# Kernel optimization log

Measured on AMD Instinct MI355X. Metric: run time of the kernel, lower is better.

## Reference

```python
import jax, jax.numpy as jnp
import numpy as np

LOWER = 300  # hidden size of the critic MLP


def setup_inputs() -> dict:
    key = jax.random.key(0)
    ks = jax.random.split(key, 6)
    N, XD, YD = 1024, 768, 768
    x = jax.random.normal(ks[0], (N, XD), dtype=jnp.float32)
    y = jax.random.normal(ks[1], (N, YD), dtype=jnp.float32)
    # Linear(x_dim+y_dim -> LOWER), Linear(LOWER -> 1); Kaiming-uniform-ish init
    b1_lim = 1.0 / np.sqrt(XD + YD)
    b2_lim = 1.0 / np.sqrt(LOWER)
    W1 = jax.random.uniform(ks[2], (XD + YD, LOWER), jnp.float32, -b1_lim, b1_lim)
    b1 = jax.random.uniform(ks[3], (LOWER,), jnp.float32, -b1_lim, b1_lim)
    W2 = jax.random.uniform(ks[4], (LOWER, 1), jnp.float32, -b2_lim, b2_lim)
    b2 = jax.random.uniform(ks[5], (1,), jnp.float32, -b2_lim, b2_lim)
    return {"x_samples": x, "y_samples": y, "W1": W1, "b1": b1, "W2": W2, "b2": b2}


def reference(x_samples, y_samples, W1, b1, W2, b2):
    N = y_samples.shape[0]
    xd = x_samples.shape[-1]
    # Decompose first Linear: cat([x, y]) @ W1 == x @ W1[:xd] + y @ W1[xd:]
    Wx, Wy = W1[:xd], W1[xd:]
    hx = x_samples @ Wx          # [N, LOWER]
    hy = y_samples @ Wy          # [N, LOWER]
    w2 = W2[:, 0]                # [LOWER]

    def critic(h):
        # relu -> Linear(LOWER->1) -> softplus
        return jax.nn.softplus(jax.nn.relu(h) @ w2 + b2[0])

    # T0[i] = F(x[i], y[i])
    T0 = critic(hx + hy + b1)                       # [N]
    # T1[i, j] = F(x[j], y[i])  (x tiled over dim 0, y over dim 1)
    h_pair = hy[:, None, :] + hx[None, :, :] + b1   # [N, N, LOWER]
    T1 = critic(h_pair)                             # [N, N]
    lower_bound = (T0.mean()
                   - jax.nn.logsumexp(T1, axis=1).mean()
                   - jnp.log(jnp.float32(N)))
    return lower_bound
```

## Files before the change

### kernel.cpp

```cpp
#include <hip/hip_runtime.h>
#include <math.h>

#define N_S 1024
#define XD  768
#define LOW 300
#define KP  320
#define KP2 160

typedef _Float16 h2  __attribute__((ext_vector_type(2)));
typedef __fp16   g2  __attribute__((ext_vector_type(2)));
typedef _Float16 v8h __attribute__((ext_vector_type(8)));
typedef float    f4  __attribute__((ext_vector_type(4)));

union U32H2 { unsigned int u; h2 h; };
__device__ inline h2 u2h(unsigned int v){ U32H2 t; t.u = v; return t.h; }
__device__ inline unsigned int pk(float a, float b){
    g2 t = __builtin_amdgcn_cvt_pkrtz(a, b);
    return __builtin_bit_cast(unsigned int, t);
}
union U4V8 { uint4 u; v8h v; };

#define STR 34

__global__ __launch_bounds__(512)
void gemm_h(const float* __restrict__ x, const float* __restrict__ y,
            const float* __restrict__ W1, const float* __restrict__ b1g,
            _Float16* __restrict__ hx_h, _Float16* __restrict__ hy_h)
{
    const int which = blockIdx.z;
    const float* A = which ? y : x;
    const float* W = W1 + (size_t)which * XD * LOW;
    _Float16* out = which ? hy_h : hx_h;

    const int n0 = blockIdx.x * 64;
    const int r0 = blockIdx.y * 64;

    __shared__ unsigned int As[2][64][STR];
    __shared__ unsigned int Bs[2][64][STR];

    const int tid = threadIdx.x;
    const int w = tid >> 6, l = tid & 63;
    const int wn = w >> 1, wm = w & 1;
    const int lr = l & 15, lg = l >> 4;

    const int arow = tid >> 3, aq = tid & 7;
    const int bn = tid & 63, bms = tid >> 6;
    const bool bin = (n0 + bn) < LOW;

    f4 acc[2] = {};

    float4 a0, a1; float bw[8];
    a0 = *(const float4*)&A[(size_t)(r0 + arow) * XD + aq * 8];
    a1 = *(const float4*)&A[(size_t)(r0 + arow) * XD + aq * 8 + 4];
    #pragma unroll
    for (int s = 0; s < 8; ++s)
        bw[s] = bin ? W[(size_t)(bms * 8 + s) * LOW + n0 + bn] : 0.f;

    const int NC = XD / 64;
    for (int c = 0; c < NC; ++c) {
        const int buf = c & 1;
        {
            uint4 pa = { pk(a0.x,a0.y), pk(a0.z,a0.w), pk(a1.x,a1.y), pk(a1.z,a1.w) };
            *(uint4*)&As[buf][arow][aq * 4] = pa;
            uint4 pb = { pk(bw[0],bw[1]), pk(bw[2],bw[3]), pk(bw[4],bw[5]), pk(bw[6],bw[7]) };
            *(uint4*)&Bs[buf][bn][bms * 4] = pb;
        }
        __syncthreads();
        if (c + 1 < NC) {
            const int kb = (c + 1) * 64;
            a0 = *(const float4*)&A[(size_t)(r0 + arow) * XD + kb + aq * 8];
            a1 = *(const float4*)&A[(size_t)(r0 + arow) * XD + kb + aq * 8 + 4];
            #pragma unroll
            for (int s = 0; s < 8; ++s)
                bw[s] = bin ? W[(size_t)(kb + bms * 8 + s) * LOW + n0 + bn] : 0.f;
        }
        #pragma unroll
        for (int ks = 0; ks < 2; ++ks) {
            const int ko = ks * 16 + lg * 4;
            U4V8 bf; bf.u = *(const uint4*)&Bs[buf][wn * 16 + lr][ko];
            #pragma unroll
            for (int mt = 0; mt < 2; ++mt) {
                U4V8 af; af.u = *(const uint4*)&As[buf][wm * 32 + mt * 16 + lr][ko];
                acc[mt] = __builtin_amdgcn_mfma_f32_16x16x32_f16(af.v, bf.v, acc[mt], 0, 0, 0);
            }
        }
    }

    const int col = n0 + wn * 16 + lr;
    const float b1v = (which && col < LOW) ? b1g[col] : 0.f;
    #pragma unroll
    for (int mt = 0; mt < 2; ++mt)
        #pragma unroll
        for (int r = 0; r < 4; ++r) {
            const int row = r0 + wm * 32 + mt * 16 + lg * 4 + r;
            out[(size_t)row * KP + col] = (_Float16)(acc[mt][r] + b1v);
        }
}

__global__ __launch_bounds__(256)
void pair_kernel(const unsigned int* __restrict__ hx_h, const unsigned int* __restrict__ hy_h,
                 const float* __restrict__ W2, const float* __restrict__ b2,
                 float* __restrict__ part, float* __restrict__ diag)
{
    const int j0 = blockIdx.x * 64;
    const int i0 = blockIdx.y * 32;
    const int jb = blockIdx.x;

    __shared__ unsigned int Hy[2][16][36];
    __shared__ unsigned int Hx[2][16][66];
    __shared__ unsigned int w2s[KP2];

    const int tid = threadIdx.x;
    const int tx = tid & 31;
    const int ty = tid >> 5;

    if (tid < KP2) {
        int k = tid * 2;
        float w0 = (k < LOW) ? W2[k] : 0.f;
        float w1 = (k + 1 < LOW) ? W2[k + 1] : 0.f;
        U32H2 p; p.h = h2{(_Float16)w0, (_Float16)w1};
        w2s[tid] = p.u;
    }

    const int yi = tid >> 3, yq = tid & 7;
    const int xj = tid >> 2, xq = tid & 3;

    uint2 ga  = *(const uint2*)&hy_h[(size_t)(i0 + yi) * KP2 + 2 * yq];
    uint2 gb0 = *(const uint2*)&hx_h[(size_t)(j0 + xj) * KP2 + 4 * xq];
    uint2 gb1 = *(const uint2*)&hx_h[(size_t)(j0 + xj) * KP2 + 4 * xq + 2];

    float acc[4][2] = {};
    const h2 hz = h2{(_Float16)0.f, (_Float16)0.f};

    const int NC = KP2 / 16;
    for (int c = 0; c < NC; ++c) {
        const int buf = c & 1;
        Hy[buf][2 * yq][yi]     = ga.x;
        Hy[buf][2 * yq + 1][yi] = ga.y;
        Hx[buf][4 * xq][xj]     = gb0.x;
        Hx[buf][4 * xq + 1][xj] = gb0.y;
        Hx[buf][4 * xq + 2][xj] = gb1.x;
        Hx[buf][4 * xq + 3][xj] = gb1.y;
        __syncthreads();
        if (c + 1 < NC) {
            const int kb = (c + 1) * 16;
            ga  = *(const uint2*)&hy_h[(size_t)(i0 + yi) * KP2 + kb + 2 * yq];
            gb0 = *(const uint2*)&hx_h[(size_t)(j0 + xj) * KP2 + kb + 4 * xq];
            gb1 = *(const uint2*)&hx_h[(size_t)(j0 + xj) * KP2 + kb + 4 * xq + 2];
        }
        #pragma unroll
        for (int kk = 0; kk < 16; ++kk) {
            const uint4 ya = *(const uint4*)&Hy[buf][kk][ty * 4];
            const uint2 xb = *(const uint2*)&Hx[buf][kk][tx * 2];
            const h2 w  = u2h(w2s[c * 16 + kk]);
            const h2 x0 = u2h(xb.x), x1 = u2h(xb.y);
            const unsigned int yar[4] = {ya.x, ya.y, ya.z, ya.w};
            #pragma unroll
            for (int r = 0; r < 4; ++r) {
                const h2 a = u2h(yar[r]);
                h2 z0 = __builtin_elementwise_max(a + x0, hz);
                h2 z1 = __builtin_elementwise_max(a + x1, hz);
                acc[r][0] = __builtin_amdgcn_fdot2(z0, w, acc[r][0], false);
                acc[r][1] = __builtin_amdgcn_fdot2(z1, w, acc[r][1], false);
            }
        }
    }

    const float b2v = b2[0];
    #pragma unroll
    for (int r = 0; r < 4; ++r) {
        const int row = i0 + ty * 4 + r;
        float s0 = acc[r][0] + b2v, s1 = acc[r][1] + b2v;
        float sp0 = fmaxf(s0, 0.f) + __logf(1.f + __expf(-fabsf(s0)));
        float sp1 = fmaxf(s1, 0.f) + __logf(1.f + __expf(-fabsf(s1)));
        const int c0 = j0 + tx * 2;
        if (c0 == row)     diag[row] = sp0;
        if (c0 + 1 == row) diag[row] = sp1;
        float es = __expf(sp0) + __expf(sp1);
        #pragma unroll
        for (int o = 1; o <= 16; o <<= 1) es += __shfl_xor(es, o, 64);
        if ((tid & 31) == 0) part[(size_t)row * 16 + jb] = es;
    }
}

__global__ __launch_bounds__(1024)
void lse_final(const float* __restrict__ part, const float* __restrict__ diag,
               float* __restrict__ out)
{
    const int i = threadIdx.x;
    const float4* p = (const float4*)(part + (size_t)i * 16);
    float s = 0.f;
    #pragma unroll
    for (int q = 0; q < 4; ++q) {
        float4 v = p[q];
        s += (v.x + v.y) + (v.z + v.w);
    }
    float c = diag[i] - __logf(s);

    #pragma unroll
    for (int o = 32; o > 0; o >>= 1) c += __shfl_xor(c, o, 64);
    __shared__ float ss[16];
    const int wid = i >> 6, lane = i & 63;
    if (lane == 0) ss[wid] = c;
    __syncthreads();
    if (i == 0) {
        float t = 0.f;
        #pragma unroll
        for (int q = 0; q < 16; ++q) t += ss[q];
        out[0] = t * (1.0f / N_S) - logf((float)N_S);
    }
}

extern "C" void kernel_launch(void* const* d_in, const int* in_sizes, int n_in,
                              void* d_out, int out_size, void* d_ws, size_t ws_size,
                              hipStream_t stream)
{
    const float* x  = (const float*)d_in[0];
    const float* y  = (const float*)d_in[1];
    const float* W1 = (const float*)d_in[2];
    const float* b1 = (const float*)d_in[3];
    const float* W2 = (const float*)d_in[4];
    const float* b2 = (const float*)d_in[5];
    float* out = (float*)d_out;

    unsigned int* hx_h = (unsigned int*)d_ws;
    unsigned int* hy_h = hx_h + (size_t)N_S * KP2;
    float* part = (float*)(hy_h + (size_t)N_S * KP2);
    float* diag = part + (size_t)N_S * 16;

    dim3 g1(5, 16, 2);
    gemm_h<<<g1, 512, 0, stream>>>(x, y, W1, b1,
                                   (_Float16*)hx_h, (_Float16*)hy_h);

    dim3 g2(16, 32);
    pair_kernel<<<g2, 256, 0, stream>>>(hx_h, hy_h, W2, b2, part, diag);

    lse_final<<<1, 1024, 0, stream>>>(part, diag, out);
}
```

Baseline: 41.85 us.

## Enlarge pair tile to 64x64 and fold softplus-exp identity into LSE

The pair kernel now computes a 64x64 output tile per block with a 4x4 register micro-tile per thread, staging hx/hy as uint2 pairs in shared memory and reading W2 directly from global into registers per chunk. It uses the identity exp(softplus(s)) = 1 + exp(s), so each element needs one exp instead of exp+log+exp, and the constant N is added back in the final reduction. Softplus is evaluated only on diagonal elements. This cuts transcendental work and raises arithmetic intensity per shared load. The cost is more register pressure from the larger tile, and fewer blocks in the grid.

```diff
diff --git a/kernel.cpp b/kernel.cpp
--- a/kernel.cpp
+++ b/kernel.cpp
@@ -97,71 +97,80 @@
         }
 }
 
+#define NCH 10
 __global__ __launch_bounds__(256)
 void pair_kernel(const unsigned int* __restrict__ hx_h, const unsigned int* __restrict__ hy_h,
                  const float* __restrict__ W2, const float* __restrict__ b2,
                  float* __restrict__ part, float* __restrict__ diag)
 {
-    const int j0 = blockIdx.x * 64;
-    const int i0 = blockIdx.y * 32;
-    const int jb = blockIdx.x;
-
-    __shared__ unsigned int Hy[2][16][36];
-    __shared__ unsigned int Hx[2][16][66];
-    __shared__ unsigned int w2s[KP2];
+    const int bx = blockIdx.x, by = blockIdx.y;
+    const int j0 = bx * 64, i0 = by * 64;
+
+    __shared__ uint2 Hy[2][8][68];
+    __shared__ uint2 Hx[2][8][68];
 
     const int tid = threadIdx.x;
-    const int tx = tid & 31;
-    const int ty = tid >> 5;
-
-    if (tid < KP2) {
-        int k = tid * 2;
-        float w0 = (k < LOW) ? W2[k] : 0.f;
-        float w1 = (k + 1 < LOW) ? W2[k + 1] : 0.f;
-        U32H2 p; p.h = h2{(_Float16)w0, (_Float16)w1};
-        w2s[tid] = p.u;
-    }
-
-    const int yi = tid >> 3, yq = tid & 7;
-    const int xj = tid >> 2, xq = tid & 3;
-
-    uint2 ga  = *(const uint2*)&hy_h[(size_t)(i0 + yi) * KP2 + 2 * yq];
-    uint2 gb0 = *(const uint2*)&hx_h[(size_t)(j0 + xj) * KP2 + 4 * xq];
-    uint2 gb1 = *(const uint2*)&hx_h[(size_t)(j0 + xj) * KP2 + 4 * xq + 2];
-
-    float acc[4][2] = {};
+    const int tx = tid & 15;
+    const int ty = tid >> 4;
+
+    const int srow = tid >> 2, skq = tid & 3;
+
+    const unsigned int* gy = &hy_h[(size_t)(i0 + srow) * KP2 + skq * 4];
+    const unsigned int* gx = &hx_h[(size_t)(j0 + srow) * KP2 + skq * 4];
+
+    uint4 ga = *(const uint4*)gy;
+    uint4 gb = *(const uint4*)gx;
+
+    float acc[4][4] = {};
     const h2 hz = h2{(_Float16)0.f, (_Float16)0.f};
 
-    const int NC = KP2 / 16;
-    for (int c = 0; c < NC; ++c) {
+    for (int c = 0; c < NCH; ++c) {
         const int buf = c & 1;
-        Hy[buf][2 * yq][yi]     = ga.x;
-        Hy[buf][2 * yq + 1][yi] = ga.y;
-        Hx[buf][4 * xq][xj]     = gb0.x;
-        Hx[buf][4 * xq + 1][xj] = gb0.y;
-        Hx[buf][4 * xq + 2][xj] = gb1.x;
-        Hx[buf][4 * xq + 3][xj] = gb1.y;
+        Hy[buf][skq*2  ][srow] = make_uint2(ga.x, ga.y);
+        Hy[buf][skq*2+1][srow] = make_uint2(ga.z, ga.w);
+        Hx[buf][skq*2  ][srow] = make_uint2(gb.x, gb.y);
+        Hx[buf][skq*2+1][srow] = make_uint2(gb.z, gb.w);
         __syncthreads();
-        if (c + 1 < NC) {
-            const int kb = (c + 1) * 16;
-            ga  = *(const uint2*)&hy_h[(size_t)(i0 + yi) * KP2 + kb + 2 * yq];
-            gb0 = *(const uint2*)&hx_h[(size_t)(j0 + xj) * KP2 + kb + 4 * xq];
-            gb1 = *(const uint2*)&hx_h[(size_t)(j0 + xj) * KP2 + kb + 4 * xq + 2];
-        }
-        #pragma unroll
-        for (int kk = 0; kk < 16; ++kk) {
-            const uint4 ya = *(const uint4*)&Hy[buf][kk][ty * 4];
-            const uint2 xb = *(const uint2*)&Hx[buf][kk][tx * 2];
-            const h2 w  = u2h(w2s[c * 16 + kk]);
-            const h2 x0 = u2h(xb.x), x1 = u2h(xb.y);
-            const unsigned int yar[4] = {ya.x, ya.y, ya.z, ya.w};
+        if (c + 1 < NCH) {
+            ga = *(const uint4*)(gy + (c + 1) * 16);
+            gb = *(const uint4*)(gx + (c + 1) * 16);
+        }
+
+        unsigned int wp[16];
+        {
+            const int kb = c * 32;
+            #pragma unroll
+            for (int t = 0; t < 8; ++t) {
+                float4 wv;
+                if (kb + t * 4 + 3 < LOW) wv = *(const float4*)&W2[kb + t * 4];
+                else wv = float4{0.f, 0.f, 0.f, 0.f};
+                wp[t * 2]     = pk(wv.x, wv.y);
+                wp[t * 2 + 1] = pk(wv.z, wv.w);
+            }
+        }
+
+        #pragma unroll
+        for (int kk2 = 0; kk2 < 8; ++kk2) {
+            uint2 ya[4], xb[4];
+            #pragma unroll
+            for (int r = 0; r < 4; ++r) ya[r] = Hy[buf][kk2][ty * 4 + r];
+            #pragma unroll
+            for (int q = 0; q < 4; ++q) xb[q] = Hx[buf][kk2][q * 16 + tx];
+            const h2 w0 = u2h(wp[kk2 * 2]);
+            const h2 w1 = u2h(wp[kk2 * 2 + 1]);
             #pragma unroll
             for (int r = 0; r < 4; ++r) {
-                const h2 a = u2h(yar[r]);
-                h2 z0 = __builtin_elementwise_max(a + x0, hz);
-                h2 z1 = __builtin_elementwise_max(a + x1, hz);
-                acc[r][0] = __builtin_amdgcn_fdot2(z0, w, acc[r][0], false);
-                acc[r][1] = __builtin_amdgcn_fdot2(z1, w, acc[r][1], false);
+                const h2 a0 = u2h(ya[r].x);
+                const h2 a1 = u2h(ya[r].y);
+                #pragma unroll
+                for (int q = 0; q < 4; ++q) {
+                    const h2 b0 = u2h(xb[q].x);
+                    const h2 b1 = u2h(xb[q].y);
+                    h2 z0 = __builtin_elementwise_max(a0 + b0, hz);
+                    h2 z1 = __builtin_elementwise_max(a1 + b1, hz);
+                    acc[r][q] = __builtin_amdgcn_fdot2(z0, w0, acc[r][q], false);
+                    acc[r][q] = __builtin_amdgcn_fdot2(z1, w1, acc[r][q], false);
+                }
             }
         }
     }
@@ -170,16 +179,18 @@
     #pragma unroll
     for (int r = 0; r < 4; ++r) {
         const int row = i0 + ty * 4 + r;
-        float s0 = acc[r][0] + b2v, s1 = acc[r][1] + b2v;
-        float sp0 = fmaxf(s0, 0.f) + __logf(1.f + __expf(-fabsf(s0)));
-        float sp1 = fmaxf(s1, 0.f) + __logf(1.f + __expf(-fabsf(s1)));
-        const int c0 = j0 + tx * 2;
-        if (c0 == row)     diag[row] = sp0;
-        if (c0 + 1 == row) diag[row] = sp1;
-        float es = __expf(sp0) + __expf(sp1);
-        #pragma unroll
-        for (int o = 1; o <= 16; o <<= 1) es += __shfl_xor(es, o, 64);
-        if ((tid & 31) == 0) part[(size_t)row * 16 + jb] = es;
+        float es = 0.f;
+        #pragma unroll
+        for (int q = 0; q < 4; ++q) {
+            const float s = acc[r][q] + b2v;
+            es += __expf(s);
+            const int col = j0 + q * 16 + tx;
+            if (col == row)
+                diag[row] = fmaxf(s, 0.f) + __logf(1.f + __expf(-fabsf(s)));
+        }
+        #pragma unroll
+        for (int o = 1; o <= 8; o <<= 1) es += __shfl_xor(es, o, 64);
+        if (tx == 0) part[(size_t)row * 16 + bx] = es;
     }
 }
 
@@ -195,7 +206,7 @@
         float4 v = p[q];
         s += (v.x + v.y) + (v.z + v.w);
     }
-    float c = diag[i] - __logf(s);
+    float c = diag[i] - __logf((float)N_S + s);
 
     #pragma unroll
     for (int o = 32; o > 0; o >>= 1) c += __shfl_xor(c, o, 64);
@@ -232,7 +243,7 @@
     gemm_h<<<g1, 512, 0, stream>>>(x, y, W1, b1,
                                    (_Float16*)hx_h, (_Float16*)hy_h);
 
-    dim3 g2(16, 32);
+    dim3 g2(16, 16);
     pair_kernel<<<g2, 256, 0, stream>>>(hx_h, hy_h, W2, b2, part, diag);
 
     lse_final<<<1, 1024, 0, stream>>>(part, diag, out);
```

New measurement: 44.31 us. 1.06x slower.

## Fuse GEMM, pair and LSE stages into one cooperative kernel

Applied to the files above, without the earlier changes.

Merges the three kernels into a single cooperative launch that separates the projection GEMM, pairwise critic and final reduction with grid-wide syncs, sharing LDS via a union. The GEMM is retiled to 32x64 blocks with 256 threads so all phases use the same block size. Softplus followed by exp is replaced algebraically by summing exp(s) and taking log(N + sum), removing transcendental work per pair. Risks include grid.sync overhead and, if the cooperative launch fails, a fallback three-kernel path.

```diff
diff --git a/kernel.cpp b/kernel.cpp
--- a/kernel.cpp
+++ b/kernel.cpp
@@ -1,11 +1,15 @@
 #include <hip/hip_runtime.h>
+#include <hip/hip_cooperative_groups.h>
 #include <math.h>
+
+namespace cg = cooperative_groups;
 
 #define N_S 1024
 #define XD  768
 #define LOW 300
 #define KP  320
 #define KP2 160
+#define GRID 512
 
 typedef _Float16 h2  __attribute__((ext_vector_type(2)));
 typedef __fp16   g2  __attribute__((ext_vector_type(2)));
@@ -20,27 +24,33 @@
 }
 union U4V8 { uint4 u; v8h v; };
 
-#define STR 34
-
-__global__ __launch_bounds__(512)
-void gemm_h(const float* __restrict__ x, const float* __restrict__ y,
-            const float* __restrict__ W1, const float* __restrict__ b1g,
-            _Float16* __restrict__ hx_h, _Float16* __restrict__ hy_h)
-{
-    const int which = blockIdx.z;
+struct SmemG {
+    unsigned int As[2][32][34];
+    unsigned int Bs[2][64][34];
+};
+struct SmemP {
+    unsigned int Hy[2][16][36];
+    unsigned int Hx[2][16][66];
+    unsigned int w2s[KP2];
+};
+union Smem { SmemG g; SmemP p; };
+
+__device__ void phase_gemm(Smem& sm, int job,
+    const float* __restrict__ x, const float* __restrict__ y,
+    const float* __restrict__ W1, const float* __restrict__ b1g,
+    unsigned int* __restrict__ hx_h, unsigned int* __restrict__ hy_h)
+{
+    const int tid = threadIdx.x;
+    const int which = job >= 160;
+    const int t = which ? job - 160 : job;
+    const int n0 = (t % 5) * 64;
+    const int r0 = (t / 5) * 32;
     const float* A = which ? y : x;
     const float* W = W1 + (size_t)which * XD * LOW;
-    _Float16* out = which ? hy_h : hx_h;
-
-    const int n0 = blockIdx.x * 64;
-    const int r0 = blockIdx.y * 64;
-
-    __shared__ unsigned int As[2][64][STR];
-    __shared__ unsigned int Bs[2][64][STR];
-
-    const int tid = threadIdx.x;
+    _Float16* outh = (_Float16*)(which ? hy_h : hx_h);
+
     const int w = tid >> 6, l = tid & 63;
-    const int wn = w >> 1, wm = w & 1;
+    const int wn = w & 1, wm = w >> 1;
     const int lr = l & 15, lg = l >> 4;
 
     const int arow = tid >> 3, aq = tid & 7;
@@ -48,111 +58,104 @@
     const bool bin = (n0 + bn) < LOW;
 
     f4 acc[2] = {};
-
-    float4 a0, a1; float bw[8];
+    float4 a0, a1; float bw[16];
     a0 = *(const float4*)&A[(size_t)(r0 + arow) * XD + aq * 8];
     a1 = *(const float4*)&A[(size_t)(r0 + arow) * XD + aq * 8 + 4];
     #pragma unroll
-    for (int s = 0; s < 8; ++s)
-        bw[s] = bin ? W[(size_t)(bms * 8 + s) * LOW + n0 + bn] : 0.f;
+    for (int s = 0; s < 16; ++s)
+        bw[s] = bin ? W[(size_t)(bms * 16 + s) * LOW + n0 + bn] : 0.f;
 
     const int NC = XD / 64;
     for (int c = 0; c < NC; ++c) {
         const int buf = c & 1;
-        {
-            uint4 pa = { pk(a0.x,a0.y), pk(a0.z,a0.w), pk(a1.x,a1.y), pk(a1.z,a1.w) };
-            *(uint4*)&As[buf][arow][aq * 4] = pa;
-            uint4 pb = { pk(bw[0],bw[1]), pk(bw[2],bw[3]), pk(bw[4],bw[5]), pk(bw[6],bw[7]) };
-            *(uint4*)&Bs[buf][bn][bms * 4] = pb;
-        }
+        *(uint4*)&sm.g.As[buf][arow][aq * 4] =
+            uint4{ pk(a0.x,a0.y), pk(a0.z,a0.w), pk(a1.x,a1.y), pk(a1.z,a1.w) };
+        *(uint4*)&sm.g.Bs[buf][bn][bms * 8] =
+            uint4{ pk(bw[0],bw[1]), pk(bw[2],bw[3]), pk(bw[4],bw[5]), pk(bw[6],bw[7]) };
+        *(uint4*)&sm.g.Bs[buf][bn][bms * 8 + 4] =
+            uint4{ pk(bw[8],bw[9]), pk(bw[10],bw[11]), pk(bw[12],bw[13]), pk(bw[14],bw[15]) };
         __syncthreads();
         if (c + 1 < NC) {
             const int kb = (c + 1) * 64;
             a0 = *(const float4*)&A[(size_t)(r0 + arow) * XD + kb + aq * 8];
             a1 = *(const float4*)&A[(size_t)(r0 + arow) * XD + kb + aq * 8 + 4];
             #pragma unroll
-            for (int s = 0; s < 8; ++s)
-                bw[s] = bin ? W[(size_t)(kb + bms * 8 + s) * LOW + n0 + bn] : 0.f;
+            for (int s = 0; s < 16; ++s)
+                bw[s] = bin ? W[(size_t)(kb + bms * 16 + s) * LOW + n0 + bn] : 0.f;
         }
         #pragma unroll
         for (int ks = 0; ks < 2; ++ks) {
             const int ko = ks * 16 + lg * 4;
-            U4V8 bf; bf.u = *(const uint4*)&Bs[buf][wn * 16 + lr][ko];
+            U4V8 af; af.u = *(const uint4*)&sm.g.As[buf][wm * 16 + lr][ko];
             #pragma unroll
-            for (int mt = 0; mt < 2; ++mt) {
-                U4V8 af; af.u = *(const uint4*)&As[buf][wm * 32 + mt * 16 + lr][ko];
-                acc[mt] = __builtin_amdgcn_mfma_f32_16x16x32_f16(af.v, bf.v, acc[mt], 0, 0, 0);
+            for (int nt = 0; nt < 2; ++nt) {
+                U4V8 bf; bf.u = *(const uint4*)&sm.g.Bs[buf][wn * 32 + nt * 16 + lr][ko];
+                acc[nt] = __builtin_amdgcn_mfma_f32_16x16x32_f16(af.v, bf.v, acc[nt], 0, 0, 0);
             }
         }
     }
 
-    const int col = n0 + wn * 16 + lr;
-    const float b1v = (which && col < LOW) ? b1g[col] : 0.f;
-    #pragma unroll
-    for (int mt = 0; mt < 2; ++mt)
+    #pragma unroll
+    for (int nt = 0; nt < 2; ++nt) {
+        const int col = n0 + wn * 32 + nt * 16 + lr;
+        const float b1v = (which && col < LOW) ? b1g[col] : 0.f;
         #pragma unroll
         for (int r = 0; r < 4; ++r) {
-            const int row = r0 + wm * 32 + mt * 16 + lg * 4 + r;
-            out[(size_t)row * KP + col] = (_Float16)(acc[mt][r] + b1v);
-        }
-}
-
-__global__ __launch_bounds__(256)
-void pair_kernel(const unsigned int* __restrict__ hx_h, const unsigned int* __restrict__ hy_h,
-                 const float* __restrict__ W2, const float* __restrict__ b2,
-                 float* __restrict__ part, float* __restrict__ diag)
-{
-    const int j0 = blockIdx.x * 64;
-    const int i0 = blockIdx.y * 32;
-    const int jb = blockIdx.x;
-
-    __shared__ unsigned int Hy[2][16][36];
-    __shared__ unsigned int Hx[2][16][66];
-    __shared__ unsigned int w2s[KP2];
-
+            const int row = r0 + wm * 16 + lg * 4 + r;
+            outh[(size_t)row * KP + col] = (_Float16)(acc[nt][r] + b1v);
+        }
+    }
+}
+
+__device__ void phase_pair(Smem& sm, int bid,
+    const unsigned int* __restrict__ hx_h, const unsigned int* __restrict__ hy_h,
+    const float* __restrict__ W2, const float* __restrict__ b2,
+    float* __restrict__ part, float* __restrict__ diag)
+{
     const int tid = threadIdx.x;
-    const int tx = tid & 31;
-    const int ty = tid >> 5;
+    const int jb = bid & 15, ib = bid >> 4;
+    const int j0 = jb * 64, i0 = ib * 32;
+    const int tx = tid & 31, ty = tid >> 5;
 
     if (tid < KP2) {
         int k = tid * 2;
         float w0 = (k < LOW) ? W2[k] : 0.f;
         float w1 = (k + 1 < LOW) ? W2[k + 1] : 0.f;
-        U32H2 p; p.h = h2{(_Float16)w0, (_Float16)w1};
-        w2s[tid] = p.u;
+        sm.p.w2s[tid] = pk(w0, w1);
     }
 
     const int yi = tid >> 3, yq = tid & 7;
     const int xj = tid >> 2, xq = tid & 3;
 
-    uint2 ga  = *(const uint2*)&hy_h[(size_t)(i0 + yi) * KP2 + 2 * yq];
-    uint2 gb0 = *(const uint2*)&hx_h[(size_t)(j0 + xj) * KP2 + 4 * xq];
-    uint2 gb1 = *(const uint2*)&hx_h[(size_t)(j0 + xj) * KP2 + 4 * xq + 2];
+    const unsigned int* gy = &hy_h[(size_t)(i0 + yi) * KP2 + 2 * yq];
+    const unsigned int* gx = &hx_h[(size_t)(j0 + xj) * KP2 + 4 * xq];
+    uint2 ga  = *(const uint2*)gy;
+    uint2 gb0 = *(const uint2*)gx;
+    uint2 gb1 = *(const uint2*)(gx + 2);
 
     float acc[4][2] = {};
     const h2 hz = h2{(_Float16)0.f, (_Float16)0.f};
 
-    const int NC = KP2 / 16;
-    for (int c = 0; c < NC; ++c) {
+    const int NCH = KP2 / 16;
+    for (int c = 0; c < NCH; ++c) {
         const int buf = c & 1;
-        Hy[buf][2 * yq][yi]     = ga.x;
-        Hy[buf][2 * yq + 1][yi] = ga.y;
-        Hx[buf][4 * xq][xj]     = gb0.x;
-        Hx[buf][4 * xq + 1][xj] = gb0.y;
-        Hx[buf][4 * xq + 2][xj] = gb1.x;
-        Hx[buf][4 * xq + 3][xj] = gb1.y;
+        sm.p.Hy[buf][2*yq  ][yi] = ga.x;
+        sm.p.Hy[buf][2*yq+1][yi] = ga.y;
+        sm.p.Hx[buf][4*xq  ][xj] = gb0.x;
+        sm.p.Hx[buf][4*xq+1][xj] = gb0.y;
+        sm.p.Hx[buf][4*xq+2][xj] = gb1.x;
+        sm.p.Hx[buf][4*xq+3][xj] = gb1.y;
         __syncthreads();
-        if (c + 1 < NC) {
-            const int kb = (c + 1) * 16;
-            ga  = *(const uint2*)&hy_h[(size_t)(i0 + yi) * KP2 + kb + 2 * yq];
-            gb0 = *(const uint2*)&hx_h[(size_t)(j0 + xj) * KP2 + kb + 4 * xq];
-            gb1 = *(const uint2*)&hx_h[(size_t)(j0 + xj) * KP2 + kb + 4 * xq + 2];
+        if (c + 1 < NCH) {
+            ga  = *(const uint2*)(gy + (c + 1) * 16);
+            gb0 = *(const uint2*)(gx + (c + 1) * 16);
+            gb1 = *(const uint2*)(gx + (c + 1) * 16 + 2);
         }
         #pragma unroll
         for (int kk = 0; kk < 16; ++kk) {
-            const uint4 ya = *(const uint4*)&Hy[buf][kk][ty * 4];
-            const uint2 xb = *(const uint2*)&Hx[buf][kk][tx * 2];
-            const h2 w  = u2h(w2s[c * 16 + kk]);
+            const uint4 ya = *(const uint4*)&sm.p.Hy[buf][kk][ty * 4];
+            const uint2 xb = *(const uint2*)&sm.p.Hx[buf][kk][tx * 2];
+            const h2 w  = u2h(sm.p.w2s[c * 16 + kk]);
             const h2 x0 = u2h(xb.x), x1 = u2h(xb.y);
             const unsigned int yar[4] = {ya.x, ya.y, ya.z, ya.w};
             #pragma unroll
@@ -171,44 +174,85 @@
     for (int r = 0; r < 4; ++r) {
         const int row = i0 + ty * 4 + r;
         float s0 = acc[r][0] + b2v, s1 = acc[r][1] + b2v;
-        float sp0 = fmaxf(s0, 0.f) + __logf(1.f + __expf(-fabsf(s0)));
-        float sp1 = fmaxf(s1, 0.f) + __logf(1.f + __expf(-fabsf(s1)));
         const int c0 = j0 + tx * 2;
-        if (c0 == row)     diag[row] = sp0;
-        if (c0 + 1 == row) diag[row] = sp1;
-        float es = __expf(sp0) + __expf(sp1);
+        if (c0 == row)     diag[row] = fmaxf(s0, 0.f) + __logf(1.f + __expf(-fabsf(s0)));
+        if (c0 + 1 == row) diag[row] = fmaxf(s1, 0.f) + __logf(1.f + __expf(-fabsf(s1)));
+        float es = __expf(s0) + __expf(s1);
         #pragma unroll
         for (int o = 1; o <= 16; o <<= 1) es += __shfl_xor(es, o, 64);
-        if ((tid & 31) == 0) part[(size_t)row * 16 + jb] = es;
-    }
-}
-
-__global__ __launch_bounds__(1024)
-void lse_final(const float* __restrict__ part, const float* __restrict__ diag,
-               float* __restrict__ out)
-{
-    const int i = threadIdx.x;
-    const float4* p = (const float4*)(part + (size_t)i * 16);
-    float s = 0.f;
-    #pragma unroll
-    for (int q = 0; q < 4; ++q) {
-        float4 v = p[q];
-        s += (v.x + v.y) + (v.z + v.w);
-    }
-    float c = diag[i] - __logf(s);
-
-    #pragma unroll
-    for (int o = 32; o > 0; o >>= 1) c += __shfl_xor(c, o, 64);
-    __shared__ float ss[16];
-    const int wid = i >> 6, lane = i & 63;
-    if (lane == 0) ss[wid] = c;
+        if (tx == 0) part[(size_t)row * 16 + jb] = es;
+    }
+}
+
+__device__ void phase_lse(const float* __restrict__ part,
+                          const float* __restrict__ diag, float* __restrict__ out)
+{
+    __shared__ float ssum[4];
+    const int tid = threadIdx.x;
+    float csum = 0.f;
+    #pragma unroll
+    for (int g = 0; g < 4; ++g) {
+        const int row = g * 256 + tid;
+        const float4* p = (const float4*)(part + (size_t)row * 16);
+        float s = 0.f;
+        #pragma unroll
+        for (int q = 0; q < 4; ++q) {
+            float4 v = p[q];
+            s += (v.x + v.y) + (v.z + v.w);
+        }
+        csum += diag[row] - __logf((float)N_S + s);
+    }
+    #pragma unroll
+    for (int o = 32; o > 0; o >>= 1) csum += __shfl_xor(csum, o, 64);
+    if ((tid & 63) == 0) ssum[tid >> 6] = csum;
     __syncthreads();
-    if (i == 0) {
-        float t = 0.f;
-        #pragma unroll
-        for (int q = 0; q < 16; ++q) t += ss[q];
-        out[0] = t * (1.0f / N_S) - logf((float)N_S);
-    }
+    if (tid == 0)
+        out[0] = (ssum[0] + ssum[1] + ssum[2] + ssum[3]) * (1.0f / N_S)
+               - logf((float)N_S);
+}
+
+__global__ __launch_bounds__(256)
+void fused(const float* __restrict__ x, const float* __restrict__ y,
+           const float* __restrict__ W1, const float* __restrict__ b1g,
+           const float* __restrict__ W2, const float* __restrict__ b2,
+           unsigned int* __restrict__ hx_h, unsigned int* __restrict__ hy_h,
+           float* __restrict__ part, float* __restrict__ diag,
+           float* __restrict__ out)
+{
+    __shared__ Smem sm;
+    cg::grid_group grid = cg::this_grid();
+    const int bid = blockIdx.x;
+
+    if (bid < 320)
+        phase_gemm(sm, bid, x, y, W1, b1g, hx_h, hy_h);
+    grid.sync();
+    phase_pair(sm, bid, hx_h, hy_h, W2, b2, part, diag);
+    grid.sync();
+    if (bid == 0)
+        phase_lse(part, diag, out);
+}
+
+__global__ __launch_bounds__(256)
+void gemm_k(const float* __restrict__ x, const float* __restrict__ y,
+            const float* __restrict__ W1, const float* __restrict__ b1g,
+            unsigned int* __restrict__ hx_h, unsigned int* __restrict__ hy_h)
+{
+    __shared__ Smem sm;
+    phase_gemm(sm, blockIdx.x, x, y, W1, b1g, hx_h, hy_h);
+}
+__global__ __launch_bounds__(256)
+void pair_k(const unsigned int* __restrict__ hx_h, const unsigned int* __restrict__ hy_h,
+            const float* __restrict__ W2, const float* __restrict__ b2,
+            float* __restrict__ part, float* __restrict__ diag)
+{
+    __shared__ Smem sm;
+    phase_pair(sm, blockIdx.x, hx_h, hy_h, W2, b2, part, diag);
+}
+__global__ __launch_bounds__(256)
+void lse_k(const float* __restrict__ part, const float* __restrict__ diag,
+           float* __restrict__ out)
+{
+    phase_lse(part, diag, out);
 }
 
 extern "C" void kernel_launch(void* const* d_in, const int* in_sizes, int n_in,
@@ -221,19 +265,23 @@
     const float* b1 = (const float*)d_in[3];
     const float* W2 = (const float*)d_in[4];
     const float* b2 = (const float*)d_in[5];
-    float* out = (float*)d_out;
+    float* outp = (float*)d_out;
 
     unsigned int* hx_h = (unsigned int*)d_ws;
     unsigned int* hy_h = hx_h + (size_t)N_S * KP2;
     float* part = (float*)(hy_h + (size_t)N_S * KP2);
     float* diag = part + (size_t)N_S * 16;
 
-    dim3 g1(5, 16, 2);
-    gemm_h<<<g1, 512, 0, stream>>>(x, y, W1, b1,
-                                   (_Float16*)hx_h, (_Float16*)hy_h);
-
-    dim3 g2(16, 32);
-    pair_kernel<<<g2, 256, 0, stream>>>(hx_h, hy_h, W2, b2, part, diag);
-
-    lse_final<<<1, 1024, 0, stream>>>(part, diag, out);
-}
+    void* args[] = { (void*)&x, (void*)&y, (void*)&W1, (void*)&b1,
+                     (void*)&W2, (void*)&b2, (void*)&hx_h, (void*)&hy_h,
+                     (void*)&part, (void*)&diag, (void*)&outp };
+
+    hipError_t err = hipLaunchCooperativeKernel((const void*)fused,
+                                                dim3(GRID), dim3(256),
+                                                args, 0, stream);
+    if (err != hipSuccess) {
+        gemm_k<<<320, 256, 0, stream>>>(x, y, W1, b1, hx_h, hy_h);
+        pair_k<<<512, 256, 0, stream>>>(hx_h, hy_h, W2, b2, part, diag);
+        lse_k<<<1, 256, 0, stream>>>(part, diag, outp);
+    }
+}
```

New measurement: 166.2 us. 3.97x slower.
